# Performance work log

Measured on AMD Instinct MI355X. Metric: run time of the kernel, lower is better.

The kernel has to match this reference:

```python
import jax, jax.numpy as jnp
import numpy as np

WZ, WH, WW = 2, 6, 12
WIN = WZ * WH * WW  # 144
DEPTH, DIM, HEADS = 2, 192, 6
NEG = -1e9


def earth_position_index():
    zi = np.arange(WZ); zj = -np.arange(WZ) * WZ
    hi = np.arange(WH); hj = -np.arange(WH) * WH
    w = np.arange(WW)
    c1 = np.stack(np.meshgrid(zi, hi, w, indexing='ij')).reshape(3, -1)
    c2 = np.stack(np.meshgrid(zj, hj, w, indexing='ij')).reshape(3, -1)
    coords = (c1[:, :, None] - c2[:, None, :]).transpose(1, 2, 0).copy()
    coords[:, :, 2] += WW - 1
    coords[:, :, 1] *= 2 * WW - 1
    coords[:, :, 0] *= (2 * WW - 1) * WH * WH
    return jnp.asarray(coords.sum(-1))


def shift_mask(Z, H):
    # Swin-style mask over Z (vertical) and H (latitude); W (longitude) is circular.
    sz, sh = WZ // 2, WH // 2
    region = np.zeros((Z, H), np.int32)
    cnt = 0
    for zs in (slice(0, Z - WZ), slice(Z - WZ, Z - sz), slice(Z - sz, Z)):
        for hs in (slice(0, H - WH), slice(H - WH, H - sh), slice(H - sh, H)):
            region[zs, hs] = cnt; cnt += 1
    r = region.reshape(Z // WZ, WZ, H // WH, WH).transpose(0, 2, 1, 3).reshape(-1, WZ * WH)
    r = np.repeat(r, WW, axis=1)  # window token order is (z,h,w)
    m = np.where(r[:, :, None] == r[:, None, :], 0.0, NEG).astype(np.float32)
    return jnp.asarray(m)


def window_partition(x, Z, H, W):
    B, C = x.shape[0], x.shape[-1]
    x = x.reshape(B, Z // WZ, WZ, H // WH, WH, W // WW, WW, C)
    x = x.transpose(0, 1, 3, 5, 2, 4, 6, 7)
    return x.reshape(B, (Z // WZ) * (H // WH) * (W // WW), WIN, C)


def window_reverse(xw, Z, H, W):
    B, C = xw.shape[0], xw.shape[-1]
    x = xw.reshape(B, Z // WZ, H // WH, W // WW, WZ, WH, WW, C)
    x = x.transpose(0, 1, 4, 2, 5, 3, 6, 7)
    return x.reshape(B, Z, H, W, C)


def layernorm(x, g, b):
    mu = x.mean(-1, keepdims=True)
    var = jnp.mean((x - mu) ** 2, axis=-1, keepdims=True)
    return (x - mu) * jax.lax.rsqrt(var + 1e-5) * g + b


def attn_windows(xw, qkv_w, qkv_b, proj_w, proj_b, bias_tab, pos_idx, mask):
    B, nW, N, C = xw.shape
    hd = C // HEADS
    qkv = (xw @ qkv_w + qkv_b).reshape(B, nW, N, 3, HEADS, hd)
    q, k, v = qkv[..., 0, :, :], qkv[..., 1, :, :], qkv[..., 2, :, :]
    attn = jnp.einsum('bwnhd,bwmhd->bwhnm', q * (hd ** -0.5), k)
    bias = bias_tab[pos_idx]
    attn = attn + bias.transpose(2, 0, 1)[None, None]
    if mask is not None:
        nzh = mask.shape[0]
        attn = attn.reshape(B, nzh, nW // nzh, HEADS, N, N) + mask[None, :, None, None]
        attn = attn.reshape(B, nW, HEADS, N, N)
    attn = jax.nn.softmax(attn, axis=-1)
    out = jnp.einsum('bwhnm,bwmhd->bwnhd', attn, v).reshape(B, nW, N, C)
    return out @ proj_w + proj_b


def forward(x, qkv_w, qkv_b, proj_w, proj_b, bias_tab,
            ln1_g, ln1_b, ln2_g, ln2_b, mlp_w1, mlp_b1, mlp_w2, mlp_b2, Z, H, W):
    B, L, C = x.shape
    pos_idx = earth_position_index()
    mask = shift_mask(Z, H)
    depth = qkv_w.shape[0]
    for i in range(depth):
        roll = (i % 2 == 1)
        shortcut = x
        xg = x.reshape(B, Z, H, W, C)
        if roll:
            xg = jnp.roll(xg, (-(WZ // 2), -(WH // 2), -(WW // 2)), axis=(1, 2, 3))
        xw = window_partition(xg, Z, H, W)
        xw = attn_windows(xw, qkv_w[i], qkv_b[i], proj_w[i], proj_b[i],
                          bias_tab[i], pos_idx, mask if roll else None)
        xg = window_reverse(xw, Z, H, W)
        if roll:
            xg = jnp.roll(xg, (WZ // 2, WH // 2, WW // 2), axis=(1, 2, 3))
        xa = xg.reshape(B, L, C)
        x = shortcut + layernorm(xa, ln1_g[i], ln1_b[i])
        h = jax.nn.gelu(x @ mlp_w1[i] + mlp_b1[i], approximate=False)
        h = h @ mlp_w2[i] + mlp_b2[i]
        x = x + layernorm(h, ln2_g[i], ln2_b[i])
    return x


def setup_inputs() -> dict:
    key = jax.random.key(0)
    ks = jax.random.split(key, 16)
    B, Z, H, W, C = 1, 8, 96, 180, DIM
    L = Z * H * W
    bias_rows = (2 * WW - 1) * WH * WH * WZ * WZ  # 3312
    s = 0.02
    return {
        'x': jax.random.normal(ks[0], (B, L, C), jnp.float32),
        'qkv_w': jax.random.normal(ks[1], (DEPTH, C, 3 * C), jnp.float32) * s,
        'qkv_b': jnp.zeros((DEPTH, 3 * C), jnp.float32),
        'proj_w': jax.random.normal(ks[2], (DEPTH, C, C), jnp.float32) * s,
        'proj_b': jnp.zeros((DEPTH, C), jnp.float32),
        'bias_tab': jax.random.normal(ks[3], (DEPTH, bias_rows, HEADS), jnp.float32) * s,
        'ln1_g': jnp.ones((DEPTH, C), jnp.float32),
        'ln1_b': jnp.zeros((DEPTH, C), jnp.float32),
        'ln2_g': jnp.ones((DEPTH, C), jnp.float32),
        'ln2_b': jnp.zeros((DEPTH, C), jnp.float32),
        'mlp_w1': jax.random.normal(ks[4], (DEPTH, C, 4 * C), jnp.float32) * s,
        'mlp_b1': jnp.zeros((DEPTH, 4 * C), jnp.float32),
        'mlp_w2': jax.random.normal(ks[5], (DEPTH, 4 * C, C), jnp.float32) * s,
        'mlp_b2': jnp.zeros((DEPTH, C), jnp.float32),
        'Z': Z, 'H': H, 'W': W,
    }


def reference(x, qkv_w, qkv_b, proj_w, proj_b, bias_tab, ln1_g, ln1_b, ln2_g, ln2_b,
              mlp_w1, mlp_b1, mlp_w2, mlp_b2, Z, H, W):
    return forward(x, qkv_w, qkv_b, proj_w, proj_b, bias_tab, ln1_g, ln1_b,
                   ln2_g, ln2_b, mlp_w1, mlp_b1, mlp_w2, mlp_b2, Z, H, W)
```

## Files before the change

kernel.cpp:

```cpp
#include <hip/hip_runtime.h>
#include <hip/hip_bf16.h>
#include <math.h>

#define L_TOK 138240
#define NW 960

typedef __attribute__((ext_vector_type(8))) short s16x8;
typedef __attribute__((ext_vector_type(8))) unsigned short u16x8;
typedef __attribute__((ext_vector_type(4))) unsigned short u16x4;
typedef __attribute__((ext_vector_type(4))) float f32x4;

__device__ __forceinline__ float bf2f(unsigned short u){
  union{unsigned int u;float f;} v; v.u=((unsigned int)u)<<16; return v.f;
}
__device__ __forceinline__ unsigned short f2bf(float f){
  __hip_bfloat16 b = __float2bfloat16(f);
  union { __hip_bfloat16 b; unsigned short u; } v; v.b = b; return v.u;
}
__device__ __forceinline__ void gll16(const void* g, void* l) {
  __builtin_amdgcn_global_load_lds((const __attribute__((address_space(1))) void*)g,
                                   (__attribute__((address_space(3))) void*)l, 16, 0, 0);
}
__device__ __forceinline__ float gelu_f(float v){
  const float s = v * 0.70710678118654752f;
  const float a = fabsf(s);
  const float t = 1.0f / (1.0f + 0.3275911f * a);
  float p = 1.061405429f;
  p = p*t - 1.453152027f;
  p = p*t + 1.421413741f;
  p = p*t - 0.284496736f;
  p = p*t + 0.254829592f;
  p = p*t;
  float y = 1.0f - p * __expf(-a*a);
  y = copysignf(y, s);
  return 0.5f * v * (1.0f + y);
}

template<int MODE, int NTILES, int BM>
__global__ __launch_bounds__(256) void gemm_rowblk(
    const float* __restrict__ A,
    const unsigned short* __restrict__ Bt,
    const float* __restrict__ bias,
    unsigned short* __restrict__ out)
{
  __shared__ unsigned short As[BM][200];
  const int tid = threadIdx.x;
  const int wid = tid >> 6, lane = tid & 63;
  const int lr = lane & 15, kg = lane >> 4;
  const int bm = blockIdx.x;
  constexpr int NI = (BM == 128) ? 2 : 1;
  const int wm = (BM == 128) ? (wid >> 1) * 64 : 0;
  const int wn = (BM == 128) ? (wid & 1) * 32 : wid * 16;
  const int N = NTILES * 64;

  constexpr int NCH = BM * 48 / 256;
  #pragma unroll
  for (int i = 0; i < NCH; i++) {
    const int c = tid + i*256;
    const int r = c / 48, p = c % 48;
    const float4 v = *(const float4*)&A[(size_t)(bm*BM + r)*192 + p*4];
    u16x4 t; t[0]=f2bf(v.x); t[1]=f2bf(v.y); t[2]=f2bf(v.z); t[3]=f2bf(v.w);
    *(u16x4*)&As[r][p*4] = t;
  }
  __syncthreads();

  s16x8 a[4][6];
  #pragma unroll
  for (int mi = 0; mi < 4; mi++)
    #pragma unroll
    for (int ks = 0; ks < 6; ks++)
      a[mi][ks] = *(const s16x8*)&As[wm + mi*16 + lr][ks*32 + kg*8];

  for (int bn = 0; bn < NTILES; bn++) {
    s16x8 b[NI][6];
    #pragma unroll
    for (int ni = 0; ni < NI; ni++)
      #pragma unroll
      for (int ks = 0; ks < 6; ks++)
        b[ni][ks] = *(const s16x8*)&Bt[(size_t)(bn*64 + wn + ni*16 + lr)*192 + ks*32 + kg*8];

    f32x4 acc[4][NI] = {};
    #pragma unroll
    for (int ks = 0; ks < 6; ks++)
      #pragma unroll
      for (int mi = 0; mi < 4; mi++)
        #pragma unroll
        for (int ni = 0; ni < NI; ni++)
          acc[mi][ni] = __builtin_amdgcn_mfma_f32_16x16x32_bf16(a[mi][ks], b[ni][ks], acc[mi][ni], 0, 0, 0);

    #pragma unroll
    for (int mi = 0; mi < 4; mi++) {
      #pragma unroll
      for (int ni = 0; ni < NI; ni++) {
        const int col = bn*64 + wn + ni*16 + lr;
        const float bv = bias[col];
        #pragma unroll
        for (int q = 0; q < 4; q++) {
          const int row = bm*BM + wm + mi*16 + kg*4 + q;
          float v = acc[mi][ni][q] + bv;
          if (MODE == 1) v = gelu_f(v);
          out[(size_t)row*N + col] = f2bf(v);
        }
      }
    }
  }
}

__global__ __launch_bounds__(256) void gemm_ln(
    const unsigned short* __restrict__ A,
    const unsigned short* __restrict__ Bt,
    const float* __restrict__ bias, const float* __restrict__ g,
    const float* __restrict__ bta,
    float* __restrict__ x,
    int row0, int K)
{
  __shared__ unsigned short As[2][128*32];
  __shared__ unsigned short Bs[2][192*32];
  __shared__ float rowstat[128][2][2];
  const int tid = threadIdx.x;
  const int wid = tid >> 6, lane = tid & 63;
  const int lr = lane & 15, kg = lane >> 4;
  const int bm = blockIdx.x;
  const int wm = (wid >> 1) * 64, wn = (wid & 1) * 96;
  const int rsub = lane >> 2, kc = lane & 3;

  f32x4 acc[4][6] = {};
  const int nst = K / 32;

  #pragma unroll
  for (int i = 0; i < 2; i++)
    gll16(&A[(size_t)(bm*128 + wid*32 + i*16 + rsub)*K + kc*8], &As[0][(wid*32 + i*16)*32]);
  #pragma unroll
  for (int j = 0; j < 3; j++)
    gll16(&Bt[(size_t)(wid*48 + j*16 + rsub)*K + kc*8], &Bs[0][(wid*48 + j*16)*32]);
  __syncthreads();

  for (int t = 0; t < nst; t++) {
    const int cur = t & 1, nxt = cur ^ 1;
    if (t + 1 < nst) {
      const int k1 = (t+1)*32;
      #pragma unroll
      for (int i = 0; i < 2; i++)
        gll16(&A[(size_t)(bm*128 + wid*32 + i*16 + rsub)*K + k1 + kc*8], &As[nxt][(wid*32 + i*16)*32]);
      #pragma unroll
      for (int j = 0; j < 3; j++)
        gll16(&Bt[(size_t)(wid*48 + j*16 + rsub)*K + k1 + kc*8], &Bs[nxt][(wid*48 + j*16)*32]);
    }
    s16x8 a[4], b[6];
    #pragma unroll
    for (int mi = 0; mi < 4; mi++) a[mi] = *(const s16x8*)&As[cur][(wm + mi*16 + lr)*32 + kg*8];
    #pragma unroll
    for (int ni = 0; ni < 6; ni++) b[ni] = *(const s16x8*)&Bs[cur][(wn + ni*16 + lr)*32 + kg*8];
    #pragma unroll
    for (int mi = 0; mi < 4; mi++)
      #pragma unroll
      for (int ni = 0; ni < 6; ni++)
        acc[mi][ni] = __builtin_amdgcn_mfma_f32_16x16x32_bf16(a[mi], b[ni], acc[mi][ni], 0, 0, 0);
    __syncthreads();
  }

  float bv[6], gv[6], btv[6];
  #pragma unroll
  for (int ni = 0; ni < 6; ni++) {
    const int col = wn + ni*16 + lr;
    bv[ni] = bias[col]; gv[ni] = g[col]; btv[ni] = bta[col];
  }
  #pragma unroll
  for (int mi = 0; mi < 4; mi++) {
    float s[4] = {0,0,0,0}, ss[4] = {0,0,0,0};
    #pragma unroll
    for (int ni = 0; ni < 6; ni++)
      #pragma unroll
      for (int q = 0; q < 4; q++) {
        const float v = acc[mi][ni][q] + bv[ni];
        s[q] += v; ss[q] += v*v;
      }
    #pragma unroll
    for (int q = 0; q < 4; q++) {
      #pragma unroll
      for (int m = 1; m < 16; m <<= 1) {
        s[q]  += __shfl_xor(s[q],  m, 64);
        ss[q] += __shfl_xor(ss[q], m, 64);
      }
    }
    if (lr == 0) {
      #pragma unroll
      for (int q = 0; q < 4; q++) {
        const int r = wm + mi*16 + kg*4 + q;
        rowstat[r][wid & 1][0] = s[q];
        rowstat[r][wid & 1][1] = ss[q];
      }
    }
  }
  __syncthreads();
  #pragma unroll
  for (int mi = 0; mi < 4; mi++) {
    #pragma unroll
    for (int q = 0; q < 4; q++) {
      const int rl = wm + mi*16 + kg*4 + q;
      const float s  = rowstat[rl][0][0] + rowstat[rl][1][0];
      const float ss = rowstat[rl][0][1] + rowstat[rl][1][1];
      const float mu = s * (1.0f/192.0f);
      const float rs = rsqrtf(ss * (1.0f/192.0f) - mu*mu + 1e-5f);
      const size_t grow = (size_t)(row0 + bm*128 + rl) * 192;
      #pragma unroll
      for (int ni = 0; ni < 6; ni++) {
        const float v = acc[mi][ni][q] + bv[ni];
        const float o = (v - mu) * rs * gv[ni] + btv[ni];
        x[grow + wn + ni*16 + lr] += o;
      }
    }
  }
}

__global__ __launch_bounds__(256) void fused_mlp(
    const float* __restrict__ xr,
    const unsigned short* __restrict__ W1t,
    const unsigned short* __restrict__ W2t,
    const float* __restrict__ b1, const float* __restrict__ b2,
    const float* __restrict__ g, const float* __restrict__ bt,
    float* __restrict__ x)
{
  __shared__ unsigned short As[64][200];
  __shared__ unsigned short Hs[2][64][72];
  __shared__ float rowstat[64][4][2];
  const int tid = threadIdx.x, wid = tid >> 6, lane = tid & 63;
  const int lr = lane & 15, kg = lane >> 4;
  const int row0 = blockIdx.x * 64;

  #pragma unroll
  for (int i = 0; i < 12; i++) {
    const int c = tid + i*256;
    const int r = c / 48, p = c % 48;
    const float4 v = *(const float4*)&xr[(size_t)(row0 + r)*192 + p*4];
    u16x4 t; t[0]=f2bf(v.x); t[1]=f2bf(v.y); t[2]=f2bf(v.z); t[3]=f2bf(v.w);
    *(u16x4*)&As[r][p*4] = t;
  }
  __syncthreads();

  f32x4 yacc[4][3] = {};
  for (int t = 0; t < 12; t++) {
    const int hb = t & 1;
    s16x8 w1f[6];
    #pragma unroll
    for (int ks = 0; ks < 6; ks++)
      w1f[ks] = *(const s16x8*)&W1t[(size_t)(t*64 + wid*16 + lr)*192 + ks*32 + kg*8];
    const float4 b1q = *(const float4*)&b1[t*64 + wid*16 + kg*4];
    #pragma unroll
    for (int mb = 0; mb < 4; mb++) {
      f32x4 hacc = {0.f, 0.f, 0.f, 0.f};
      #pragma unroll
      for (int ks = 0; ks < 6; ks++) {
        const s16x8 xf = *(const s16x8*)&As[mb*16 + lr][ks*32 + kg*8];
        hacc = __builtin_amdgcn_mfma_f32_16x16x32_bf16(w1f[ks], xf, hacc, 0, 0, 0);
      }
      u16x4 hv;
      hv[0] = f2bf(gelu_f(hacc[0] + b1q.x));
      hv[1] = f2bf(gelu_f(hacc[1] + b1q.y));
      hv[2] = f2bf(gelu_f(hacc[2] + b1q.z));
      hv[3] = f2bf(gelu_f(hacc[3] + b1q.w));
      *(u16x4*)&Hs[hb][mb*16 + lr][wid*16 + kg*4] = hv;
    }
    __syncthreads();
    #pragma unroll
    for (int kk = 0; kk < 2; kk++) {
      s16x8 b2f[3];
      #pragma unroll
      for (int nj = 0; nj < 3; nj++)
        b2f[nj] = *(const s16x8*)&W2t[(size_t)(wid*48 + nj*16 + lr)*768 + t*64 + kk*32 + kg*8];
      #pragma unroll
      for (int mi = 0; mi < 4; mi++) {
        const s16x8 a2 = *(const s16x8*)&Hs[hb][mi*16 + lr][kk*32 + kg*8];
        #pragma unroll
        for (int nj = 0; nj < 3; nj++)
          yacc[mi][nj] = __builtin_amdgcn_mfma_f32_16x16x32_bf16(a2, b2f[nj], yacc[mi][nj], 0, 0, 0);
      }
    }
  }

  float bv[3], gv[3], btv[3];
  #pragma unroll
  for (int nj = 0; nj < 3; nj++) {
    const int col = wid*48 + nj*16 + lr;
    bv[nj] = b2[col]; gv[nj] = g[col]; btv[nj] = bt[col];
  }
  #pragma unroll
  for (int mi = 0; mi < 4; mi++) {
    float s[4] = {0,0,0,0}, ss[4] = {0,0,0,0};
    #pragma unroll
    for (int nj = 0; nj < 3; nj++)
      #pragma unroll
      for (int q = 0; q < 4; q++) {
        const float v = yacc[mi][nj][q] + bv[nj];
        s[q] += v; ss[q] += v*v;
      }
    #pragma unroll
    for (int q = 0; q < 4; q++) {
      #pragma unroll
      for (int m = 1; m < 16; m <<= 1) {
        s[q]  += __shfl_xor(s[q],  m, 64);
        ss[q] += __shfl_xor(ss[q], m, 64);
      }
    }
    if (lr == 0) {
      #pragma unroll
      for (int q = 0; q < 4; q++) {
        rowstat[mi*16 + kg*4 + q][wid][0] = s[q];
        rowstat[mi*16 + kg*4 + q][wid][1] = ss[q];
      }
    }
  }
  __syncthreads();
  #pragma unroll
  for (int mi = 0; mi < 4; mi++) {
    #pragma unroll
    for (int q = 0; q < 4; q++) {
      const int rl = mi*16 + kg*4 + q;
      const float s  = rowstat[rl][0][0] + rowstat[rl][1][0] + rowstat[rl][2][0] + rowstat[rl][3][0];
      const float ss = rowstat[rl][0][1] + rowstat[rl][1][1] + rowstat[rl][2][1] + rowstat[rl][3][1];
      const float mu = s * (1.0f/192.0f);
      const float rs = rsqrtf(ss * (1.0f/192.0f) - mu*mu + 1e-5f);
      const size_t grow = (size_t)(row0 + rl) * 192;
      #pragma unroll
      for (int nj = 0; nj < 3; nj++) {
        const float v = yacc[mi][nj][q] + bv[nj];
        const float o = (v - mu) * rs * gv[nj] + btv[nj];
        x[grow + wid*48 + nj*16 + lr] += o;
      }
    }
  }
}

__global__ __launch_bounds__(384) void attn_win6(
    const unsigned short* __restrict__ qkv,
    const unsigned short* __restrict__ biasbt,
    unsigned short* __restrict__ attn_out,
    int roll)
{
  __shared__ unsigned short Pw[6][16][168];
  __shared__ int lmap[144];

  const int w = blockIdx.x;
  const int tid = threadIdx.x, wid = tid / 64, lane = tid & 63;
  const int lr = lane & 15, kg = lane >> 4;
  const int ww = w % 15, hw = (w / 15) % 16, zw = w / 240;

  if (tid < 144) {
    const int z1 = tid / 72, h1 = (tid % 72) / 12, w1 = tid % 12;
    int z = zw*2 + z1, h = hw*6 + h1, xx = ww*12 + w1;
    if (roll) { z = (z + 1) & 7; h = (h + 3) % 96; xx = (xx + 6) % 180; }
    lmap[tid] = (z*96 + h)*180 + xx;
  }
  __syncthreads();

  const unsigned short* bb;
  if (roll) {
    const int c = ((zw == 3) ? 2 : 0) | ((hw == 15) ? 1 : 0);
    bb = biasbt + (size_t)c*124416 + (size_t)wid*20736;
  } else {
    bb = biasbt + (size_t)wid*20736;
  }

  s16x8 kfr[9];
  #pragma unroll
  for (int ti = 0; ti < 9; ti++)
    kfr[ti] = *(const s16x8*)&qkv[(size_t)lmap[ti*16 + lr]*576 + 192 + wid*32 + kg*8];

  s16x8 vbr[2][5];
  #pragma unroll
  for (int ci = 0; ci < 2; ci++)
    #pragma unroll
    for (int ks = 0; ks < 5; ks++) {
      u16x8 t;
      #pragma unroll
      for (int j = 0; j < 8; j++) {
        const int tok = ks*32 + kg*8 + j;
        t[j] = (tok < 144) ? qkv[(size_t)lmap[tok]*576 + 384 + wid*32 + ci*16 + lr] : (unsigned short)0;
      }
      vbr[ci][ks] = (s16x8)t;
    }

  #pragma unroll
  for (int j = 0; j < 4; j++) Pw[wid][lr][144 + kg*4 + j] = 0;

  for (int s = 0; s < 9; s++) {
    const s16x8 bq = *(const s16x8*)&qkv[(size_t)lmap[s*16 + lr]*576 + wid*32 + kg*8];

    float pb[9][4];
    float mx = -3.0e38f;
    #pragma unroll
    for (int ti = 0; ti < 9; ti++) {
      f32x4 acc = {0.f, 0.f, 0.f, 0.f};
      acc = __builtin_amdgcn_mfma_f32_16x16x32_bf16(kfr[ti], bq, acc, 0, 0, 0);
      const u16x4 b4 = *(const u16x4*)&bb[(size_t)(s*9 + ti)*256 + lr*16 + kg*4];
      #pragma unroll
      for (int q = 0; q < 4; q++) {
        const float sv = acc[q] + bf2f(b4[q]);
        pb[ti][q] = sv;
        mx = fmaxf(mx, sv);
      }
    }
    mx = fmaxf(mx, __shfl_xor(mx, 16, 64));
    mx = fmaxf(mx, __shfl_xor(mx, 32, 64));

    float sum = 0.f;
    #pragma unroll
    for (int ti = 0; ti < 9; ti++)
      #pragma unroll
      for (int q = 0; q < 4; q++) {
        const float p = __expf(pb[ti][q] - mx);
        pb[ti][q] = p;
        sum += p;
      }
    sum += __shfl_xor(sum, 16, 64);
    sum += __shfl_xor(sum, 32, 64);
    const float inv = 1.0f / sum;

    #pragma unroll
    for (int ti = 0; ti < 9; ti++)
      #pragma unroll
      for (int q = 0; q < 4; q++)
        Pw[wid][lr][ti*16 + kg*4 + q] = f2bf(pb[ti][q] * inv);

    #pragma unroll
    for (int ci = 0; ci < 2; ci++) {
      f32x4 accO = {0.f, 0.f, 0.f, 0.f};
      #pragma unroll
      for (int ks = 0; ks < 5; ks++) {
        const s16x8 pa = *(const s16x8*)&Pw[wid][lr][ks*32 + kg*8];
        accO = __builtin_amdgcn_mfma_f32_16x16x32_bf16(pa, vbr[ci][ks], accO, 0, 0, 0);
      }
      #pragma unroll
      for (int q = 0; q < 4; q++) {
        const int row = s*16 + kg*4 + q;
        attn_out[(size_t)lmap[row]*192 + wid*32 + ci*16 + lr] = f2bf(accO[q]);
      }
    }
  }
}

__global__ void init_x(const float* __restrict__ xin, float* __restrict__ x, int n) {
  const int i = blockIdx.x*256 + threadIdx.x;
  if (i < n) x[i] = xin[i];
}
__global__ void copy_diag(const float* __restrict__ a, float* __restrict__ o, int n) {
  const int i = blockIdx.x*256 + threadIdx.x;
  if (i < n) o[i] = a[i] + 50.0f;
}
__global__ void transpose_w(const float* __restrict__ src, unsigned short* __restrict__ dst,
                            int K, int N, int nscale, float factor) {
  const int i = blockIdx.x*256 + threadIdx.x;
  const int tot = K*N;
  if (i >= 2*tot) return;
  const int l = i / tot, e = i % tot;
  const int k = e / N, n = e % N;
  float v = src[i];
  if (n < nscale) v *= factor;
  dst[(size_t)l*tot + (size_t)n*K + k] = f2bf(v);
}
__global__ void scale_qb(const float* __restrict__ src, float* __restrict__ dst) {
  const int i = blockIdx.x*256 + threadIdx.x;
  if (i >= 2*576) return;
  const float f = (i % 576) < 192 ? 0.17677669529663687f : 1.0f;
  dst[i] = src[i] * f;
}
__global__ void build_biasb6(const float* __restrict__ tab, unsigned short* __restrict__ bm) {
  const int i = blockIdx.x*256 + threadIdx.x;
  const int TAB = 6*144*144;
  if (i >= 5*TAB) return;
  const int tau = i / TAB, r = i % TAB;
  const int hd = r / 20736, rr = r % 20736;
  const int s = rr / 2304, rrr = rr % 2304;
  const int ti = rrr / 256, e = rrr % 256;
  const int lr_ = e / 16, c4 = e % 16;
  const int q = s*16 + lr_, tok = ti*16 + c4;
  const int z1 = q/72,  h1 = (q%72)/12,  w1 = q%12;
  const int z2 = tok/72, h2 = (tok%72)/12, w2 = tok%12;
  const int idx = (z1 + 2*z2)*828 + (h1 + 6*h2)*23 + (w1 - w2 + 11);
  const int l = (tau == 0) ? 0 : 1;
  float v = tab[(size_t)l*3312*6 + (size_t)idx*6 + hd];
  if (tau >= 1) {
    const int c = tau - 1, zs = c >> 1, hs = c & 1;
    const int rq = (zs ? (1 + z1) : 0)*3 + (hs ? (1 + (h1 >= 3)) : 0);
    const int rt = (zs ? (1 + z2) : 0)*3 + (hs ? (1 + (h2 >= 3)) : 0);
    if (rq != rt) v -= 1.0e9f;
  }
  bm[i] = f2bf(v);
}

extern "C" void kernel_launch(void* const* d_in, const int* in_sizes, int n_in,
                              void* d_out, int out_size, void* d_ws, size_t ws_size,
                              hipStream_t stream) {
  const float* x_in    = (const float*)d_in[0];
  const float* qkv_w   = (const float*)d_in[1];
  const float* qkv_b   = (const float*)d_in[2];
  const float* proj_w  = (const float*)d_in[3];
  const float* proj_b  = (const float*)d_in[4];
  const float* bias_tab= (const float*)d_in[5];
  const float* ln1_g   = (const float*)d_in[6];
  const float* ln1_b   = (const float*)d_in[7];
  const float* ln2_g   = (const float*)d_in[8];
  const float* ln2_b   = (const float*)d_in[9];
  const float* mlp_w1  = (const float*)d_in[10];
  const float* mlp_b1  = (const float*)d_in[11];
  const float* mlp_w2  = (const float*)d_in[12];
  const float* mlp_b2  = (const float*)d_in[13];

  const int nElem = L_TOK * 192;
  float* xf = (float*)d_out;

  const size_t sz_R0 = 159252480;
  const size_t sz_R1 = 53084160;
  const size_t sz_wT = 1769472;
  const size_t sz_bb = 2488320;
  const size_t sz_qb = 4608;
  const size_t need  = sz_R0 + sz_R1 + sz_wT + sz_bb + sz_qb;

  if (ws_size < need) {
    copy_diag<<<dim3((nElem+255)/256), 256, 0, stream>>>(x_in, xf, nElem);
    return;
  }

  char* ws = (char*)d_ws;
  unsigned short* R0    = (unsigned short*)(ws);
  unsigned short* R1    = (unsigned short*)(ws + sz_R0);
  unsigned short* wT    = (unsigned short*)(ws + sz_R0 + sz_R1);
  unsigned short* biasb = (unsigned short*)(ws + sz_R0 + sz_R1 + sz_wT);
  float*          qb2   = (float*)(ws + sz_R0 + sz_R1 + sz_wT + sz_bb);

  unsigned short* wT_qkv  = wT;
  unsigned short* wT_proj = wT + 221184;
  unsigned short* wT_m1   = wT + 294912;
  unsigned short* wT_m2   = wT + 589824;

  transpose_w<<<dim3((2*192*576+255)/256), 256, 0, stream>>>(qkv_w,  wT_qkv, 192, 576, 192, 0.17677669529663687f);
  transpose_w<<<dim3((2*192*192+255)/256), 256, 0, stream>>>(proj_w, wT_proj,192, 192, 0, 1.0f);
  transpose_w<<<dim3((2*192*768+255)/256), 256, 0, stream>>>(mlp_w1, wT_m1,  192, 768, 0, 1.0f);
  transpose_w<<<dim3((2*768*192+255)/256), 256, 0, stream>>>(mlp_w2, wT_m2,  768, 192, 0, 1.0f);
  build_biasb6<<<dim3((5*6*144*144+255)/256), 256, 0, stream>>>(bias_tab, biasb);
  scale_qb<<<dim3(5), 256, 0, stream>>>(qkv_b, qb2);

  init_x<<<dim3((nElem+255)/256), 256, 0, stream>>>(x_in, xf, nElem);

  for (int i = 0; i < 2; i++) {
    gemm_rowblk<0, 9, 64><<<dim3(2160), 256, 0, stream>>>(
        xf, wT_qkv + (size_t)i*110592, qb2 + i*576, R0);
    attn_win6<<<dim3(NW), 384, 0, stream>>>(
        R0, biasb + (i ? 124416 : 0), R1, i & 1);
    gemm_ln<<<dim3(1080), 256, 0, stream>>>(
        R1, wT_proj + (size_t)i*36864, proj_b + i*192,
        ln1_g + i*192, ln1_b + i*192, xf, 0, 192);
    fused_mlp<<<dim3(2160), 256, 0, stream>>>(
        xf, wT_m1 + (size_t)i*147456, wT_m2 + (size_t)i*147456,
        mlp_b1 + i*768, mlp_b2 + i*192,
        ln2_g + i*192, ln2_b + i*192, xf);
  }
}
```

Baseline: 1.013 ms.

## Keep bf16 residual copy, async-load swizzled LDS tiles, write attention in place

The residual-update epilogues now also write a bf16 copy of x. The QKV GEMM and MLP read this copy through direct global-to-LDS loads into an XOR-swizzled layout, instead of reading fp32 and converting. Attention writes its output in place into the Q slice of the qkv buffer, and the projection GEMM reads it with stride 576, which removes the separate R1 buffer. This cuts fp32 read traffic and conversion work, at the cost of an extra bf16 store in each epilogue. The in-place overwrite is only safe if each window reads its Q before writing.

```diff
diff --git a/kernel.cpp b/kernel.cpp
--- a/kernel.cpp
+++ b/kernel.cpp
@@ -36,31 +36,27 @@
   return 0.5f * v * (1.0f + y);
 }
 
-template<int MODE, int NTILES, int BM>
-__global__ __launch_bounds__(256) void gemm_rowblk(
-    const float* __restrict__ A,
+template<int NTILES>
+__global__ __launch_bounds__(256) void gemm_qkv(
+    const unsigned short* __restrict__ xb,
     const unsigned short* __restrict__ Bt,
     const float* __restrict__ bias,
     unsigned short* __restrict__ out)
 {
-  __shared__ unsigned short As[BM][200];
+  __shared__ unsigned short As[64*192];
   const int tid = threadIdx.x;
   const int wid = tid >> 6, lane = tid & 63;
   const int lr = lane & 15, kg = lane >> 4;
   const int bm = blockIdx.x;
-  constexpr int NI = (BM == 128) ? 2 : 1;
-  const int wm = (BM == 128) ? (wid >> 1) * 64 : 0;
-  const int wn = (BM == 128) ? (wid & 1) * 32 : wid * 16;
+  const int wn = wid * 16;
   const int N = NTILES * 64;
 
-  constexpr int NCH = BM * 48 / 256;
-  #pragma unroll
-  for (int i = 0; i < NCH; i++) {
+  #pragma unroll
+  for (int i = 0; i < 6; i++) {
     const int c = tid + i*256;
-    const int r = c / 48, p = c % 48;
-    const float4 v = *(const float4*)&A[(size_t)(bm*BM + r)*192 + p*4];
-    u16x4 t; t[0]=f2bf(v.x); t[1]=f2bf(v.y); t[2]=f2bf(v.z); t[3]=f2bf(v.w);
-    *(u16x4*)&As[r][p*4] = t;
+    const int r = c / 24, s = c % 24;
+    const int sg = (s & 24) | ((s ^ r) & 7);
+    gll16(&xb[(size_t)(bm*64 + r)*192 + sg*8], &As[c*8]);
   }
   __syncthreads();
 
@@ -68,41 +64,32 @@
   #pragma unroll
   for (int mi = 0; mi < 4; mi++)
     #pragma unroll
+    for (int ks = 0; ks < 6; ks++) {
+      const int m = mi*16 + lr, g = ks*4 + kg;
+      const int sg = (g & 24) | ((g ^ m) & 7);
+      a[mi][ks] = *(const s16x8*)&As[m*192 + sg*8];
+    }
+
+  for (int bn = 0; bn < NTILES; bn++) {
+    s16x8 b[6];
+    #pragma unroll
     for (int ks = 0; ks < 6; ks++)
-      a[mi][ks] = *(const s16x8*)&As[wm + mi*16 + lr][ks*32 + kg*8];
-
-  for (int bn = 0; bn < NTILES; bn++) {
-    s16x8 b[NI][6];
-    #pragma unroll
-    for (int ni = 0; ni < NI; ni++)
-      #pragma unroll
-      for (int ks = 0; ks < 6; ks++)
-        b[ni][ks] = *(const s16x8*)&Bt[(size_t)(bn*64 + wn + ni*16 + lr)*192 + ks*32 + kg*8];
-
-    f32x4 acc[4][NI] = {};
+      b[ks] = *(const s16x8*)&Bt[(size_t)(bn*64 + wn + lr)*192 + ks*32 + kg*8];
+    f32x4 acc[4] = {};
     #pragma unroll
     for (int ks = 0; ks < 6; ks++)
       #pragma unroll
       for (int mi = 0; mi < 4; mi++)
-        #pragma unroll
-        for (int ni = 0; ni < NI; ni++)
-          acc[mi][ni] = __builtin_amdgcn_mfma_f32_16x16x32_bf16(a[mi][ks], b[ni][ks], acc[mi][ni], 0, 0, 0);
-
-    #pragma unroll
-    for (int mi = 0; mi < 4; mi++) {
-      #pragma unroll
-      for (int ni = 0; ni < NI; ni++) {
-        const int col = bn*64 + wn + ni*16 + lr;
-        const float bv = bias[col];
-        #pragma unroll
-        for (int q = 0; q < 4; q++) {
-          const int row = bm*BM + wm + mi*16 + kg*4 + q;
-          float v = acc[mi][ni][q] + bv;
-          if (MODE == 1) v = gelu_f(v);
-          out[(size_t)row*N + col] = f2bf(v);
-        }
-      }
-    }
+        acc[mi] = __builtin_amdgcn_mfma_f32_16x16x32_bf16(a[mi][ks], b[ks], acc[mi], 0, 0, 0);
+    const int col = bn*64 + wn + lr;
+    const float bv = bias[col];
+    #pragma unroll
+    for (int mi = 0; mi < 4; mi++)
+      #pragma unroll
+      for (int q = 0; q < 4; q++) {
+        const int row = bm*64 + mi*16 + kg*4 + q;
+        out[(size_t)row*N + col] = f2bf(acc[mi][q] + bv);
+      }
   }
 }
 
@@ -111,8 +98,8 @@
     const unsigned short* __restrict__ Bt,
     const float* __restrict__ bias, const float* __restrict__ g,
     const float* __restrict__ bta,
-    float* __restrict__ x,
-    int row0, int K)
+    float* __restrict__ x, unsigned short* __restrict__ xbo,
+    int lda)
 {
   __shared__ unsigned short As[2][128*32];
   __shared__ unsigned short Bs[2][192*32];
@@ -123,13 +110,14 @@
   const int bm = blockIdx.x;
   const int wm = (wid >> 1) * 64, wn = (wid & 1) * 96;
   const int rsub = lane >> 2, kc = lane & 3;
+  const int K = 192;
 
   f32x4 acc[4][6] = {};
   const int nst = K / 32;
 
   #pragma unroll
   for (int i = 0; i < 2; i++)
-    gll16(&A[(size_t)(bm*128 + wid*32 + i*16 + rsub)*K + kc*8], &As[0][(wid*32 + i*16)*32]);
+    gll16(&A[(size_t)(bm*128 + wid*32 + i*16 + rsub)*lda + kc*8], &As[0][(wid*32 + i*16)*32]);
   #pragma unroll
   for (int j = 0; j < 3; j++)
     gll16(&Bt[(size_t)(wid*48 + j*16 + rsub)*K + kc*8], &Bs[0][(wid*48 + j*16)*32]);
@@ -141,7 +129,7 @@
       const int k1 = (t+1)*32;
       #pragma unroll
       for (int i = 0; i < 2; i++)
-        gll16(&A[(size_t)(bm*128 + wid*32 + i*16 + rsub)*K + k1 + kc*8], &As[nxt][(wid*32 + i*16)*32]);
+        gll16(&A[(size_t)(bm*128 + wid*32 + i*16 + rsub)*lda + k1 + kc*8], &As[nxt][(wid*32 + i*16)*32]);
       #pragma unroll
       for (int j = 0; j < 3; j++)
         gll16(&Bt[(size_t)(wid*48 + j*16 + rsub)*K + k1 + kc*8], &Bs[nxt][(wid*48 + j*16)*32]);
@@ -202,45 +190,49 @@
       const float ss = rowstat[rl][0][1] + rowstat[rl][1][1];
       const float mu = s * (1.0f/192.0f);
       const float rs = rsqrtf(ss * (1.0f/192.0f) - mu*mu + 1e-5f);
-      const size_t grow = (size_t)(row0 + bm*128 + rl) * 192;
+      const size_t grow = (size_t)(bm*128 + rl) * 192;
       #pragma unroll
       for (int ni = 0; ni < 6; ni++) {
         const float v = acc[mi][ni][q] + bv[ni];
         const float o = (v - mu) * rs * gv[ni] + btv[ni];
-        x[grow + wn + ni*16 + lr] += o;
+        const size_t idx = grow + wn + ni*16 + lr;
+        const float xn = x[idx] + o;
+        x[idx] = xn; xbo[idx] = f2bf(xn);
       }
     }
   }
 }
 
 __global__ __launch_bounds__(256) void fused_mlp(
-    const float* __restrict__ xr,
+    const unsigned short* __restrict__ xb,
     const unsigned short* __restrict__ W1t,
     const unsigned short* __restrict__ W2t,
     const float* __restrict__ b1, const float* __restrict__ b2,
     const float* __restrict__ g, const float* __restrict__ bt,
-    float* __restrict__ x)
+    float* __restrict__ x, unsigned short* __restrict__ xbo)
 {
-  __shared__ unsigned short As[64][200];
-  __shared__ unsigned short Hs[2][64][72];
+  __shared__ unsigned short As[64*192];
+  __shared__ unsigned short Hs[2][64*64];
   __shared__ float rowstat[64][4][2];
   const int tid = threadIdx.x, wid = tid >> 6, lane = tid & 63;
   const int lr = lane & 15, kg = lane >> 4;
   const int row0 = blockIdx.x * 64;
 
   #pragma unroll
-  for (int i = 0; i < 12; i++) {
+  for (int i = 0; i < 6; i++) {
     const int c = tid + i*256;
-    const int r = c / 48, p = c % 48;
-    const float4 v = *(const float4*)&xr[(size_t)(row0 + r)*192 + p*4];
-    u16x4 t; t[0]=f2bf(v.x); t[1]=f2bf(v.y); t[2]=f2bf(v.z); t[3]=f2bf(v.w);
-    *(u16x4*)&As[r][p*4] = t;
+    const int r = c / 24, s = c % 24;
+    const int sg = (s & 24) | ((s ^ r) & 7);
+    gll16(&xb[(size_t)(row0 + r)*192 + sg*8], &As[c*8]);
   }
   __syncthreads();
+
+  char* const hs0 = (char*)&Hs[0][0];
+  char* const hs1 = (char*)&Hs[1][0];
 
   f32x4 yacc[4][3] = {};
   for (int t = 0; t < 12; t++) {
-    const int hb = t & 1;
+    char* const hb = (t & 1) ? hs1 : hs0;
     s16x8 w1f[6];
     #pragma unroll
     for (int ks = 0; ks < 6; ks++)
@@ -248,18 +240,22 @@
     const float4 b1q = *(const float4*)&b1[t*64 + wid*16 + kg*4];
     #pragma unroll
     for (int mb = 0; mb < 4; mb++) {
+      const int m = mb*16 + lr;
       f32x4 hacc = {0.f, 0.f, 0.f, 0.f};
       #pragma unroll
       for (int ks = 0; ks < 6; ks++) {
-        const s16x8 xf = *(const s16x8*)&As[mb*16 + lr][ks*32 + kg*8];
-        hacc = __builtin_amdgcn_mfma_f32_16x16x32_bf16(w1f[ks], xf, hacc, 0, 0, 0);
+        const int gsl = ks*4 + kg;
+        const int sg = (gsl & 24) | ((gsl ^ m) & 7);
+        const s16x8 xf8 = *(const s16x8*)&As[m*192 + sg*8];
+        hacc = __builtin_amdgcn_mfma_f32_16x16x32_bf16(w1f[ks], xf8, hacc, 0, 0, 0);
       }
       u16x4 hv;
       hv[0] = f2bf(gelu_f(hacc[0] + b1q.x));
       hv[1] = f2bf(gelu_f(hacc[1] + b1q.y));
       hv[2] = f2bf(gelu_f(hacc[2] + b1q.z));
       hv[3] = f2bf(gelu_f(hacc[3] + b1q.w));
-      *(u16x4*)&Hs[hb][mb*16 + lr][wid*16 + kg*4] = hv;
+      const int cb = wid*32 + kg*8;
+      *(u16x4*)(hb + m*128 + (cb ^ ((m & 7) << 4))) = hv;
     }
     __syncthreads();
     #pragma unroll
@@ -270,7 +266,9 @@
         b2f[nj] = *(const s16x8*)&W2t[(size_t)(wid*48 + nj*16 + lr)*768 + t*64 + kk*32 + kg*8];
       #pragma unroll
       for (int mi = 0; mi < 4; mi++) {
-        const s16x8 a2 = *(const s16x8*)&Hs[hb][mi*16 + lr][kk*32 + kg*8];
+        const int m = mi*16 + lr;
+        const int cb2 = kk*64 + kg*16;
+        const s16x8 a2 = *(const s16x8*)(hb + m*128 + (cb2 ^ ((m & 7) << 4)));
         #pragma unroll
         for (int nj = 0; nj < 3; nj++)
           yacc[mi][nj] = __builtin_amdgcn_mfma_f32_16x16x32_bf16(a2, b2f[nj], yacc[mi][nj], 0, 0, 0);
@@ -325,16 +323,17 @@
       for (int nj = 0; nj < 3; nj++) {
         const float v = yacc[mi][nj][q] + bv[nj];
         const float o = (v - mu) * rs * gv[nj] + btv[nj];
-        x[grow + wid*48 + nj*16 + lr] += o;
-      }
-    }
-  }
-}
-
-__global__ __launch_bounds__(384) void attn_win6(
-    const unsigned short* __restrict__ qkv,
+        const size_t idx = grow + wid*48 + nj*16 + lr;
+        const float xn = x[idx] + o;
+        x[idx] = xn; xbo[idx] = f2bf(xn);
+      }
+    }
+  }
+}
+
+__global__ __launch_bounds__(384) void attn_win7(
+    unsigned short* qkv,
     const unsigned short* __restrict__ biasbt,
-    unsigned short* __restrict__ attn_out,
     int roll)
 {
   __shared__ unsigned short Pw[6][16][168];
@@ -433,15 +432,16 @@
       #pragma unroll
       for (int q = 0; q < 4; q++) {
         const int row = s*16 + kg*4 + q;
-        attn_out[(size_t)lmap[row]*192 + wid*32 + ci*16 + lr] = f2bf(accO[q]);
-      }
-    }
-  }
-}
-
-__global__ void init_x(const float* __restrict__ xin, float* __restrict__ x, int n) {
+        qkv[(size_t)lmap[row]*576 + wid*32 + ci*16 + lr] = f2bf(accO[q]);
+      }
+    }
+  }
+}
+
+__global__ void init_x(const float* __restrict__ xin, float* __restrict__ x,
+                       unsigned short* __restrict__ xb, int n) {
   const int i = blockIdx.x*256 + threadIdx.x;
-  if (i < n) x[i] = xin[i];
+  if (i < n) { const float f = xin[i]; x[i] = f; xb[i] = f2bf(f); }
 }
 __global__ void copy_diag(const float* __restrict__ a, float* __restrict__ o, int n) {
   const int i = blockIdx.x*256 + threadIdx.x;
@@ -510,11 +510,11 @@
   float* xf = (float*)d_out;
 
   const size_t sz_R0 = 159252480;
-  const size_t sz_R1 = 53084160;
+  const size_t sz_xb = 53084160;
   const size_t sz_wT = 1769472;
   const size_t sz_bb = 2488320;
   const size_t sz_qb = 4608;
-  const size_t need  = sz_R0 + sz_R1 + sz_wT + sz_bb + sz_qb;
+  const size_t need  = sz_R0 + sz_xb + sz_wT + sz_bb + sz_qb;
 
   if (ws_size < need) {
     copy_diag<<<dim3((nElem+255)/256), 256, 0, stream>>>(x_in, xf, nElem);
@@ -523,10 +523,10 @@
 
   char* ws = (char*)d_ws;
   unsigned short* R0    = (unsigned short*)(ws);
-  unsigned short* R1    = (unsigned short*)(ws + sz_R0);
-  unsigned short* wT    = (unsigned short*)(ws + sz_R0 + sz_R1);
-  unsigned short* biasb = (unsigned short*)(ws + sz_R0 + sz_R1 + sz_wT);
-  float*          qb2   = (float*)(ws + sz_R0 + sz_R1 + sz_wT + sz_bb);
+  unsigned short* xb    = (unsigned short*)(ws + sz_R0);
+  unsigned short* wT    = (unsigned short*)(ws + sz_R0 + sz_xb);
+  unsigned short* biasb = (unsigned short*)(ws + sz_R0 + sz_xb + sz_wT);
+  float*          qb2   = (float*)(ws + sz_R0 + sz_xb + sz_wT + sz_bb);
 
   unsigned short* wT_qkv  = wT;
   unsigned short* wT_proj = wT + 221184;
@@ -540,19 +540,19 @@
   build_biasb6<<<dim3((5*6*144*144+255)/256), 256, 0, stream>>>(bias_tab, biasb);
   scale_qb<<<dim3(5), 256, 0, stream>>>(qkv_b, qb2);
 
-  init_x<<<dim3((nElem+255)/256), 256, 0, stream>>>(x_in, xf, nElem);
+  init_x<<<dim3((nElem+255)/256), 256, 0, stream>>>(x_in, xf, xb, nElem);
 
   for (int i = 0; i < 2; i++) {
-    gemm_rowblk<0, 9, 64><<<dim3(2160), 256, 0, stream>>>(
-        xf, wT_qkv + (size_t)i*110592, qb2 + i*576, R0);
-    attn_win6<<<dim3(NW), 384, 0, stream>>>(
-        R0, biasb + (i ? 124416 : 0), R1, i & 1);
+    gemm_qkv<9><<<dim3(2160), 256, 0, stream>>>(
+        xb, wT_qkv + (size_t)i*110592, qb2 + i*576, R0);
+    attn_win7<<<dim3(NW), 384, 0, stream>>>(
+        R0, biasb + (i ? 124416 : 0), i & 1);
     gemm_ln<<<dim3(1080), 256, 0, stream>>>(
-        R1, wT_proj + (size_t)i*36864, proj_b + i*192,
-        ln1_g + i*192, ln1_b + i*192, xf, 0, 192);
+        R0, wT_proj + (size_t)i*36864, proj_b + i*192,
+        ln1_g + i*192, ln1_b + i*192, xf, xb, 576);
     fused_mlp<<<dim3(2160), 256, 0, stream>>>(
-        xf, wT_m1 + (size_t)i*147456, wT_m2 + (size_t)i*147456,
+        xb, wT_m1 + (size_t)i*147456, wT_m2 + (size_t)i*147456,
         mlp_b1 + i*768, mlp_b2 + i*192,
-        ln2_g + i*192, ln2_b + i*192, xf);
-  }
-}
+        ln2_g + i*192, ln2_b + i*192, xf, xb);
+  }
+}
```

Measured after the change: 1.075 ms. 6.2% more time.
